# Kernel tuning notes

Measured on AMD Instinct MI355X. Metric: run time of the kernel, lower is better.

Reference implementation:

```python
import jax, jax.numpy as jnp
import numpy as np

E = 256      # embed_dim
H = 4        # num_heads
EXP = 4      # expansion_factor
B, C, R = 8, 32, 255  # batch, max_cols, rows (seq = R+1 with CLS)
LN_EPS = 1e-5


def setup_inputs() -> dict:
    key = jax.random.key(0)
    ks = jax.random.split(key, 16)
    s = 0.02
    return {
        "x": jax.random.normal(ks[0], (B, C, R, E), jnp.float32),
        "real_cols": jax.random.randint(ks[1], (B,), 0, C + 1),
        "real_rows": jax.random.randint(ks[2], (B,), 0, R + 1),
        "cls_token": jax.random.normal(ks[3], (E,), jnp.float32) * s,
        # MHA in_proj (torch packs q,k,v as (3E, E)) and out_proj
        "w_qkv": jax.random.normal(ks[4], (3 * E, E), jnp.float32) * s,
        "b_qkv": jnp.zeros((3 * E,), jnp.float32),
        "w_out": jax.random.normal(ks[5], (E, E), jnp.float32) * s,
        "b_out": jnp.zeros((E,), jnp.float32),
        # LayerNorm
        "ln_g": jnp.ones((E,), jnp.float32),
        "ln_b": jnp.zeros((E,), jnp.float32),
        # FFN: Linear(E, 4E) -> ReLU -> Linear(4E, E)
        "w1": jax.random.normal(ks[6], (EXP * E, E), jnp.float32) * s,
        "b1": jnp.zeros((EXP * E,), jnp.float32),
        "w2": jax.random.normal(ks[7], (E, EXP * E), jnp.float32) * s,
        "b2": jnp.zeros((E,), jnp.float32),
    }


def reference(x, real_cols, real_rows, cls_token, w_qkv, b_qkv, w_out, b_out,
              ln_g, ln_b, w1, b1, w2, b2):
    Bn, Cn, Rn, En = x.shape
    S = Rn + 1
    Dh = En // H
    dt = x.dtype

    # prepend CLS token to every column's row sequence -> (B, C, S, E)
    cls = jnp.broadcast_to(cls_token.astype(dt), (Bn, Cn, 1, En))
    xc = jnp.concatenate([cls, x], axis=2)

    # fused qkv projection
    qkv = jnp.einsum('bcse,fe->bcsf', xc, w_qkv.astype(dt)) + b_qkv.astype(dt)
    q, k, v = jnp.split(qkv, 3, axis=-1)
    q = q.reshape(Bn, Cn, S, H, Dh)
    k = k.reshape(Bn, Cn, S, H, Dh)
    v = v.reshape(Bn, Cn, S, H, Dh)

    scale = 1.0 / np.sqrt(Dh).astype(np.float32)
    scores = jnp.einsum('bcqhd,bckhd->bchqk', q, k) * scale  # (B,C,H,S,S)

    # key_padding_mask: position 0 (CLS) always valid; row p (1..R) valid iff p <= nrow
    pos = jnp.arange(S)
    valid = (pos[None, :] == 0) | (pos[None, :] <= real_rows[:, None])  # (B, S)
    neg = jnp.asarray(-1e9, scores.dtype)
    scores = jnp.where(valid[:, None, None, None, :], scores, neg)

    attn = jax.nn.softmax(scores, axis=-1)
    ctx = jnp.einsum('bchqk,bckhd->bcqhd', attn, v).reshape(Bn, Cn, S, En)
    mha = jnp.einsum('bcse,fe->bcsf', ctx, w_out.astype(dt)) + b_out.astype(dt)

    # LayerNorm over E
    mu = mha.mean(axis=-1, keepdims=True)
    var = ((mha - mu) ** 2).mean(axis=-1, keepdims=True)
    ln = (mha - mu) * jax.lax.rsqrt(var + LN_EPS) * ln_g.astype(dt) + ln_b.astype(dt)

    # FFN with residual from ln (out = ln + ffn(ln))
    h = jax.nn.relu(jnp.einsum('bcse,fe->bcsf', ln, w1.astype(dt)) + b1.astype(dt))
    ffn = jnp.einsum('bcsf,ef->bcse', h, w2.astype(dt)) + b2.astype(dt)
    out = ln + ffn

    # rep_mode == 'cls': take CLS position; zero out padded columns
    rep = out[:, :, 0, :]  # (B, C, E)
    col_valid = (jnp.arange(Cn)[None, :] < real_cols[:, None]).astype(dt)
    return rep * col_valid[..., None]
```

## Files before the change

### kernel.cpp

```cpp
#include <hip/hip_runtime.h>
#include <hip/hip_bf16.h>
#include <math.h>

static constexpr int kC = 32, kR = 255, kE = 256;

__device__ float g_vc[256];
__device__ float g_qw[4 * 256];
__device__ float g_s0[4];
__device__ float g_qb[4];
__device__ float g_m[256 * 4 * 4];
__device__ float g_l[256 * 4 * 4];
__device__ float g_part[256 * 4 * 4 * 256];
__device__ float g_ln[256 * 256];
__device__ float g_hact[256 * 1024];
__device__ unsigned short g_wv_bf[256 * 256];
__device__ unsigned short g_wout_bf[256 * 256];
__device__ unsigned short g_w1_bf[1024 * 256];
__device__ unsigned short g_w2_bf[256 * 1024];

__device__ inline unsigned short f2bf(float f) {
  __hip_bfloat16 h = __float2bfloat16(f);
  return __builtin_bit_cast(unsigned short, h);
}
__device__ inline float bflo(unsigned int u) { return __uint_as_float(u << 16); }
__device__ inline float bfhi(unsigned int u) { return __uint_as_float(u & 0xffff0000u); }

__global__ __launch_bounds__(256) void k_setup(const float* __restrict__ cls,
                                               const float* __restrict__ w_qkv,
                                               const float* __restrict__ b_qkv,
                                               const float* __restrict__ w_out,
                                               const float* __restrict__ w1,
                                               const float* __restrict__ w2) {
  const int t = threadIdx.x;
  if (blockIdx.x >= 4) {
    const int u = blockIdx.x - 4;
    const float* src;
    unsigned short* dst;
    size_t base;
    if (u < 64) { src = w_qkv + 512 * 256; dst = g_wv_bf; base = (size_t)u * 1024; }
    else if (u < 128) { src = w_out; dst = g_wout_bf; base = (size_t)(u - 64) * 1024; }
    else if (u < 384) { src = w1; dst = g_w1_bf; base = (size_t)(u - 128) * 1024; }
    else { src = w2; dst = g_w2_bf; base = (size_t)(u - 384) * 1024; }
    const size_t idx = base + (size_t)t * 4;
    float4 v = *(const float4*)(src + idx);
    ushort4 o;
    o.x = f2bf(v.x); o.y = f2bf(v.y); o.z = f2bf(v.z); o.w = f2bf(v.w);
    *(ushort4*)(dst + idx) = o;
    return;
  }

  const int h = blockIdx.x;
  __shared__ float clss[256], q0s[256];
  clss[t] = cls[t];
  __syncthreads();
  {
    float acc = b_qkv[t];
    const float4* wr = (const float4*)(w_qkv + (size_t)t * 256);
    const float4* c4 = (const float4*)clss;
#pragma unroll 8
    for (int e4 = 0; e4 < 64; ++e4) {
      float4 w4 = wr[e4], v4 = c4[e4];
      acc += w4.x * v4.x + w4.y * v4.y + w4.z * v4.z + w4.w * v4.w;
    }
    q0s[t] = acc;
  }
  __syncthreads();
  {
    float acc = 0.f;
#pragma unroll 8
    for (int j = 0; j < 64; ++j)
      acc += q0s[h * 64 + j] * w_qkv[(size_t)(256 + h * 64 + j) * 256 + t];
    g_qw[h * 256 + t] = acc * 0.125f;
  }
  if (t < 64) {
    const int row = 256 + h * 64 + t;
    float kc = b_qkv[row];
    const float4* wr = (const float4*)(w_qkv + (size_t)row * 256);
    const float4* c4 = (const float4*)clss;
#pragma unroll 8
    for (int e4 = 0; e4 < 64; ++e4) {
      float4 w4 = wr[e4], v4 = c4[e4];
      kc += w4.x * v4.x + w4.y * v4.y + w4.z * v4.z + w4.w * v4.w;
    }
    const float q = q0s[h * 64 + t];
    float pk = q * kc, pb = q * b_qkv[row];
#pragma unroll
    for (int m = 1; m < 64; m <<= 1) {
      pk += __shfl_xor(pk, m);
      pb += __shfl_xor(pb, m);
    }
    if (t == 0) {
      g_s0[h] = pk * 0.125f;
      g_qb[h] = pb * 0.125f;
    }
  } else if (t < 128) {
    const int f = h * 64 + (t - 64);
    const int row = 512 + f;
    float acc = b_qkv[row];
    const float4* wr = (const float4*)(w_qkv + (size_t)row * 256);
    const float4* c4 = (const float4*)clss;
#pragma unroll 8
    for (int e4 = 0; e4 < 64; ++e4) {
      float4 w4 = wr[e4], v4 = c4[e4];
      acc += w4.x * v4.x + w4.y * v4.y + w4.z * v4.z + w4.w * v4.w;
    }
    g_vc[f] = acc;
  }
}

__global__ __launch_bounds__(256) void k_attn(const float* __restrict__ x,
                                              const int* __restrict__ real_cols,
                                              const int* __restrict__ real_rows) {
  const int bc = blockIdx.x, chunk = blockIdx.y;
  const int b = bc >> 5, c = bc & 31;
  if (c >= real_cols[b]) return;
  const int rr = real_rows[b];
  const int r0 = chunk * 64;
  const int nr = min(64, rr - r0);
  if (nr <= 0) return;

  __shared__ float xs[64][260];
  __shared__ float qws[4][256];
  __shared__ float ps[4][64];
  const int t = threadIdx.x, wv = t >> 6, l = t & 63;

#pragma unroll
  for (int i = 0; i < 4; ++i) qws[i][t] = g_qw[i * 256 + t];

  const float* xb = x + ((size_t)bc * kR + r0) * kE;
  for (int r = wv; r < nr; r += 4)
    *(float4*)&xs[r][4 * l] = *(const float4*)(xb + (size_t)r * kE + 4 * l);
  __syncthreads();

  const int h = wv, row = l;
  float acc = 0.f;
  const float4* qrow = (const float4*)&qws[h][0];
  const float4* xrow = (const float4*)&xs[row][0];
#pragma unroll 8
  for (int e4 = 0; e4 < 64; ++e4) {
    float4 q4 = qrow[e4];
    float4 x4 = xrow[e4];
    acc += q4.x * x4.x + q4.y * x4.y + q4.z * x4.z + q4.w * x4.w;
  }
  float s = (row < nr) ? acc + g_qb[h] : -1e30f;
  float mx = s;
#pragma unroll
  for (int m = 1; m < 64; m <<= 1) mx = fmaxf(mx, __shfl_xor(mx, m));
  float p = (row < nr) ? __expf(s - mx) : 0.f;
  float lsum = p;
#pragma unroll
  for (int m = 1; m < 64; m <<= 1) lsum += __shfl_xor(lsum, m);
  ps[h][row] = p;
  if (l == 0) {
    g_m[(bc * 4 + chunk) * 4 + h] = mx;
    g_l[(bc * 4 + chunk) * 4 + h] = lsum;
  }
  __syncthreads();

  float a0 = 0.f, a1 = 0.f, a2 = 0.f, a3 = 0.f;
  for (int r2 = 0; r2 < nr; ++r2) {
    float xv = xs[r2][t];
    a0 += ps[0][r2] * xv;
    a1 += ps[1][r2] * xv;
    a2 += ps[2][r2] * xv;
    a3 += ps[3][r2] * xv;
  }
  float* pp = g_part + (size_t)(bc * 4 + chunk) * 4 * 256;
  pp[0 * 256 + t] = a0;
  pp[1 * 256 + t] = a1;
  pp[2 * 256 + t] = a2;
  pp[3 * 256 + t] = a3;
}

__global__ __launch_bounds__(256) void k_tail(const int* __restrict__ real_cols,
                                              const int* __restrict__ real_rows,
                                              const float* __restrict__ b_qkv,
                                              const float* __restrict__ b_out,
                                              const float* __restrict__ ln_g,
                                              const float* __restrict__ ln_b) {
  const int bc = blockIdx.x, b = bc >> 5, c = bc & 31;
  if (c >= real_cols[b]) return;
  const int rr = real_rows[b];
  const int nch = (rr + 63) >> 6;
  const int t = threadIdx.x, wv = t >> 6, l = t & 63;

  __shared__ float xb[4][256];
  __shared__ float ctxs[256];
  __shared__ float al[4][4];
  __shared__ float p0s[4];
  __shared__ float rb[2][4];

  if (t < 4) {
    const int h = t;
    const float s0 = g_s0[h];
    float M = s0;
    for (int ch = 0; ch < nch; ++ch) M = fmaxf(M, g_m[(bc * 4 + ch) * 4 + h]);
    float lt = __expf(s0 - M);
    const float w0 = lt;
    float av[4] = {0.f, 0.f, 0.f, 0.f};
    for (int ch = 0; ch < nch; ++ch) {
      float e = __expf(g_m[(bc * 4 + ch) * 4 + h] - M);
      av[ch] = e;
      lt += g_l[(bc * 4 + ch) * 4 + h] * e;
    }
    const float inv = 1.f / lt;
#pragma unroll
    for (int ch = 0; ch < 4; ++ch) al[h][ch] = av[ch] * inv;
    p0s[h] = w0 * inv;
  }
  __syncthreads();

#pragma unroll
  for (int h = 0; h < 4; ++h) {
    float a = 0.f;
    for (int ch = 0; ch < nch; ++ch)
      a += al[h][ch] * g_part[(size_t)(bc * 4 + ch) * 4 * 256 + h * 256 + t];
    xb[h][t] = a;
  }
  __syncthreads();

  {
    const int h = wv;
    const float p0 = p0s[h];
    float acc = p0 * g_vc[t] + (1.f - p0) * b_qkv[512 + t];
    const uint4* wr = (const uint4*)(g_wv_bf + (size_t)t * 256);
    const float4* v4p = (const float4*)&xb[h][0];
#pragma unroll 4
    for (int e8 = 0; e8 < 32; ++e8) {
      uint4 w = wr[e8];
      float4 a = v4p[2 * e8], bb = v4p[2 * e8 + 1];
      acc += bflo(w.x) * a.x + bfhi(w.x) * a.y + bflo(w.y) * a.z + bfhi(w.y) * a.w +
             bflo(w.z) * bb.x + bfhi(w.z) * bb.y + bflo(w.w) * bb.z + bfhi(w.w) * bb.w;
    }
    ctxs[t] = acc;
  }
  __syncthreads();

  float mh;
  {
    float acc = b_out[t];
    const uint4* wr = (const uint4*)(g_wout_bf + (size_t)t * 256);
    const float4* c4 = (const float4*)&ctxs[0];
#pragma unroll 4
    for (int e8 = 0; e8 < 32; ++e8) {
      uint4 w = wr[e8];
      float4 a = c4[2 * e8], bb = c4[2 * e8 + 1];
      acc += bflo(w.x) * a.x + bfhi(w.x) * a.y + bflo(w.y) * a.z + bfhi(w.y) * a.w +
             bflo(w.z) * bb.x + bfhi(w.z) * bb.y + bflo(w.w) * bb.z + bfhi(w.w) * bb.w;
    }
    mh = acc;
  }

  float s1 = mh, s2 = mh * mh;
#pragma unroll
  for (int m = 1; m < 64; m <<= 1) {
    s1 += __shfl_xor(s1, m);
    s2 += __shfl_xor(s2, m);
  }
  if (l == 0) {
    rb[0][wv] = s1;
    rb[1][wv] = s2;
  }
  __syncthreads();
  const float mu = (rb[0][0] + rb[0][1] + rb[0][2] + rb[0][3]) * (1.f / 256.f);
  const float msq = (rb[1][0] + rb[1][1] + rb[1][2] + rb[1][3]) * (1.f / 256.f);
  const float var = msq - mu * mu;
  g_ln[(size_t)bc * 256 + t] =
      (mh - mu) * rsqrtf(var + 1e-5f) * ln_g[t] + ln_b[t];
}

__global__ __launch_bounds__(256) void k_ffn1(const float* __restrict__ b1,
                                              const int* __restrict__ real_cols) {
  const int tok0 = blockIdx.x * 8;
  const int b = tok0 >> 5, c0 = tok0 & 31;
  if (c0 >= real_cols[b]) return;
  __shared__ float lns[8][256];
  const int t = threadIdx.x;
  const int f0 = blockIdx.y * 128;
#pragma unroll
  for (int i = 0; i < 8; ++i) lns[i][t] = g_ln[(size_t)(tok0 + i) * 256 + t];
  __syncthreads();
  const int f = f0 + (t & 127), half = t >> 7;
  const uint4* wr = (const uint4*)(g_w1_bf + (size_t)f * 256);
  const float bb = b1[f];
  float acc[4] = {bb, bb, bb, bb};
  for (int e8 = 0; e8 < 32; ++e8) {
    uint4 w = wr[e8];
    const float wv0 = bflo(w.x), wv1 = bfhi(w.x), wv2 = bflo(w.y), wv3 = bfhi(w.y);
    const float wv4 = bflo(w.z), wv5 = bfhi(w.z), wv6 = bflo(w.w), wv7 = bfhi(w.w);
#pragma unroll
    for (int k = 0; k < 4; ++k) {
      const int i = half * 4 + k;
      const float4 a = *(const float4*)&lns[i][8 * e8];
      const float4 bbv = *(const float4*)&lns[i][8 * e8 + 4];
      acc[k] += wv0 * a.x + wv1 * a.y + wv2 * a.z + wv3 * a.w +
                wv4 * bbv.x + wv5 * bbv.y + wv6 * bbv.z + wv7 * bbv.w;
    }
  }
#pragma unroll
  for (int k = 0; k < 4; ++k)
    g_hact[(size_t)(tok0 + half * 4 + k) * 1024 + f] = fmaxf(acc[k], 0.f);
}

__global__ __launch_bounds__(256) void k_ffn2(const float* __restrict__ b2,
                                              const int* __restrict__ real_cols,
                                              float* __restrict__ out) {
  const int t = threadIdx.x;
  const int tok0 = blockIdx.x * 8, e0 = blockIdx.y * 32;
  const int b = tok0 >> 5, c0 = tok0 & 31;
  const int ncols = real_cols[b];
  if (c0 >= ncols) {
    out[(size_t)(tok0 + (t >> 5)) * 256 + e0 + (t & 31)] = 0.f;
    return;
  }
  __shared__ float hs[8][1024];
#pragma unroll
  for (int i = 0; i < 8; ++i) {
#pragma unroll
    for (int j = 0; j < 4; ++j)
      hs[i][j * 256 + t] = g_hact[(size_t)(tok0 + i) * 1024 + j * 256 + t];
  }
  __syncthreads();
  const int e = e0 + (t & 31), i = t >> 5;
  const int tok = tok0 + i, c = tok & 31;
  const uint4* wr = (const uint4*)(g_w2_bf + (size_t)e * 1024);
  const float4* h4 = (const float4*)&hs[i][0];
  float acc = b2[e];
  for (int f8 = 0; f8 < 128; ++f8) {
    uint4 w = wr[f8];
    float4 a = h4[2 * f8], bb = h4[2 * f8 + 1];
    acc += bflo(w.x) * a.x + bfhi(w.x) * a.y + bflo(w.y) * a.z + bfhi(w.y) * a.w +
           bflo(w.z) * bb.x + bfhi(w.z) * bb.y + bflo(w.w) * bb.z + bfhi(w.w) * bb.w;
  }
  const float lnv = g_ln[(size_t)tok * 256 + e];
  out[(size_t)tok * 256 + e] = (c < ncols) ? (lnv + acc) : 0.f;
}

extern "C" void kernel_launch(void* const* d_in, const int* in_sizes, int n_in,
                              void* d_out, int out_size, void* d_ws, size_t ws_size,
                              hipStream_t stream) {
  const float* x = (const float*)d_in[0];
  const int* real_cols = (const int*)d_in[1];
  const int* real_rows = (const int*)d_in[2];
  const float* cls = (const float*)d_in[3];
  const float* w_qkv = (const float*)d_in[4];
  const float* b_qkv = (const float*)d_in[5];
  const float* w_out = (const float*)d_in[6];
  const float* b_out = (const float*)d_in[7];
  const float* ln_g = (const float*)d_in[8];
  const float* ln_b = (const float*)d_in[9];
  const float* w1 = (const float*)d_in[10];
  const float* b1 = (const float*)d_in[11];
  const float* w2 = (const float*)d_in[12];
  const float* b2 = (const float*)d_in[13];
  float* out = (float*)d_out;
  (void)in_sizes; (void)n_in; (void)out_size; (void)d_ws; (void)ws_size;

  k_setup<<<644, 256, 0, stream>>>(cls, w_qkv, b_qkv, w_out, w1, w2);
  k_attn<<<dim3(256, 4), 256, 0, stream>>>(x, real_cols, real_rows);
  k_tail<<<256, 256, 0, stream>>>(real_cols, real_rows, b_qkv, b_out, ln_g, ln_b);
  k_ffn1<<<dim3(32, 8), 256, 0, stream>>>(b1, real_cols);
  k_ffn2<<<dim3(32, 8), 256, 0, stream>>>(b2, real_cols, out);
}
```

Measured before the change: 185.3 us.

## Fuse setup/attn/tail into persistent ticket kernel and merge FFN stages with flags

Merges the setup, attention and tail kernels into one 1024-block kernel. Blocks prefetch their x tile, then take setup work items from an atomic ticket counter, and spin-wait on completion counters before attention. A last-arriver counter per (b,c) runs the tail. The two FFN kernels become one launch in which the ffn2 blocks spin on per-group counters written by the ffn1 blocks. This removes launch gaps and overlaps the weight casting with the x loads. It relies on all blocks being co-resident, so the spin-waits risk deadlock or stalls.

```diff
diff --git a/kernel.cpp b/kernel.cpp
--- a/kernel.cpp
+++ b/kernel.cpp
@@ -3,6 +3,13 @@
 #include <math.h>
 
 static constexpr int kC = 32, kR = 255, kE = 256;
+#define AGENT __HIP_MEMORY_SCOPE_AGENT
+
+__device__ unsigned g_ticket = 0;
+__device__ unsigned g_done_heads = 0;
+__device__ unsigned g_done_all = 0;
+__device__ unsigned g_bcnt[256];
+__device__ unsigned g_gcnt[32];
 
 __device__ float g_vc[256];
 __device__ float g_qw[4 * 256];
@@ -24,172 +31,199 @@
 }
 __device__ inline float bflo(unsigned int u) { return __uint_as_float(u << 16); }
 __device__ inline float bfhi(unsigned int u) { return __uint_as_float(u & 0xffff0000u); }
-
-__global__ __launch_bounds__(256) void k_setup(const float* __restrict__ cls,
-                                               const float* __restrict__ w_qkv,
-                                               const float* __restrict__ b_qkv,
-                                               const float* __restrict__ w_out,
-                                               const float* __restrict__ w1,
-                                               const float* __restrict__ w2) {
-  const int t = threadIdx.x;
-  if (blockIdx.x >= 4) {
-    const int u = blockIdx.x - 4;
-    const float* src;
-    unsigned short* dst;
-    size_t base;
-    if (u < 64) { src = w_qkv + 512 * 256; dst = g_wv_bf; base = (size_t)u * 1024; }
-    else if (u < 128) { src = w_out; dst = g_wout_bf; base = (size_t)(u - 64) * 1024; }
-    else if (u < 384) { src = w1; dst = g_w1_bf; base = (size_t)(u - 128) * 1024; }
-    else { src = w2; dst = g_w2_bf; base = (size_t)(u - 384) * 1024; }
-    const size_t idx = base + (size_t)t * 4;
-    float4 v = *(const float4*)(src + idx);
-    ushort4 o;
-    o.x = f2bf(v.x); o.y = f2bf(v.y); o.z = f2bf(v.z); o.w = f2bf(v.w);
-    *(ushort4*)(dst + idx) = o;
-    return;
-  }
-
-  const int h = blockIdx.x;
-  __shared__ float clss[256], q0s[256];
+__device__ inline unsigned aload(unsigned* p) {
+  return __hip_atomic_load(p, __ATOMIC_ACQUIRE, AGENT);
+}
+
+__device__ void do_head_item(int h, int t, int wv, int l, float* clss, float* q0h,
+                             float* kcs, const float* __restrict__ cls,
+                             const float* __restrict__ w_qkv,
+                             const float* __restrict__ b_qkv) {
   clss[t] = cls[t];
   __syncthreads();
-  {
-    float acc = b_qkv[t];
-    const float4* wr = (const float4*)(w_qkv + (size_t)t * 256);
-    const float4* c4 = (const float4*)clss;
-#pragma unroll 8
-    for (int e4 = 0; e4 < 64; ++e4) {
-      float4 w4 = wr[e4], v4 = c4[e4];
-      acc += w4.x * v4.x + w4.y * v4.y + w4.z * v4.z + w4.w * v4.w;
-    }
-    q0s[t] = acc;
+  const float4* c4 = (const float4*)clss;
+  for (int j = wv; j < 64; j += 4) {
+    const float4* wr = (const float4*)(w_qkv + (size_t)(h * 64 + j) * 256);
+    float4 w4 = wr[l], v4 = c4[l];
+    float a = w4.x * v4.x + w4.y * v4.y + w4.z * v4.z + w4.w * v4.w;
+#pragma unroll
+    for (int m = 1; m < 64; m <<= 1) a += __shfl_xor(a, m);
+    if (l == 0) q0h[j] = a + b_qkv[h * 64 + j];
   }
   __syncthreads();
   {
     float acc = 0.f;
 #pragma unroll 8
     for (int j = 0; j < 64; ++j)
-      acc += q0s[h * 64 + j] * w_qkv[(size_t)(256 + h * 64 + j) * 256 + t];
+      acc += q0h[j] * w_qkv[(size_t)(256 + h * 64 + j) * 256 + t];
     g_qw[h * 256 + t] = acc * 0.125f;
   }
-  if (t < 64) {
-    const int row = 256 + h * 64 + t;
-    float kc = b_qkv[row];
-    const float4* wr = (const float4*)(w_qkv + (size_t)row * 256);
-    const float4* c4 = (const float4*)clss;
-#pragma unroll 8
-    for (int e4 = 0; e4 < 64; ++e4) {
-      float4 w4 = wr[e4], v4 = c4[e4];
-      kc += w4.x * v4.x + w4.y * v4.y + w4.z * v4.z + w4.w * v4.w;
-    }
-    const float q = q0s[h * 64 + t];
-    float pk = q * kc, pb = q * b_qkv[row];
+  for (int j = wv; j < 64; j += 4) {
+    const float4* wr = (const float4*)(w_qkv + (size_t)(256 + h * 64 + j) * 256);
+    float4 w4 = wr[l], v4 = c4[l];
+    float a = w4.x * v4.x + w4.y * v4.y + w4.z * v4.z + w4.w * v4.w;
+#pragma unroll
+    for (int m = 1; m < 64; m <<= 1) a += __shfl_xor(a, m);
+    if (l == 0) kcs[j] = a + b_qkv[256 + h * 64 + j];
+  }
+  __syncthreads();
+  if (wv == 0) {
+    float q = q0h[l];
+    float pk = q * kcs[l], pb = q * b_qkv[256 + h * 64 + l];
 #pragma unroll
     for (int m = 1; m < 64; m <<= 1) {
       pk += __shfl_xor(pk, m);
       pb += __shfl_xor(pb, m);
     }
-    if (t == 0) {
+    if (l == 0) {
       g_s0[h] = pk * 0.125f;
       g_qb[h] = pb * 0.125f;
     }
-  } else if (t < 128) {
-    const int f = h * 64 + (t - 64);
-    const int row = 512 + f;
-    float acc = b_qkv[row];
-    const float4* wr = (const float4*)(w_qkv + (size_t)row * 256);
-    const float4* c4 = (const float4*)clss;
-#pragma unroll 8
-    for (int e4 = 0; e4 < 64; ++e4) {
-      float4 w4 = wr[e4], v4 = c4[e4];
-      acc += w4.x * v4.x + w4.y * v4.y + w4.z * v4.z + w4.w * v4.w;
-    }
-    g_vc[f] = acc;
-  }
-}
-
-__global__ __launch_bounds__(256) void k_attn(const float* __restrict__ x,
-                                              const int* __restrict__ real_cols,
-                                              const int* __restrict__ real_rows) {
-  const int bc = blockIdx.x, chunk = blockIdx.y;
+  }
+  for (int j = wv; j < 64; j += 4) {
+    const float4* wr = (const float4*)(w_qkv + (size_t)(512 + h * 64 + j) * 256);
+    float4 w4 = wr[l], v4 = c4[l];
+    float a = w4.x * v4.x + w4.y * v4.y + w4.z * v4.z + w4.w * v4.w;
+#pragma unroll
+    for (int m = 1; m < 64; m <<= 1) a += __shfl_xor(a, m);
+    if (l == 0) g_vc[h * 64 + j] = a + b_qkv[512 + h * 64 + j];
+  }
+}
+
+__device__ void do_cast_item(int u, int t, const float* __restrict__ w_qkv,
+                             const float* __restrict__ w_out,
+                             const float* __restrict__ w1,
+                             const float* __restrict__ w2) {
+  const float* src;
+  unsigned short* dst;
+  size_t base;
+  if (u < 64) { src = w_qkv + 512 * 256; dst = g_wv_bf; base = (size_t)u * 1024; }
+  else if (u < 128) { src = w_out; dst = g_wout_bf; base = (size_t)(u - 64) * 1024; }
+  else if (u < 384) { src = w1; dst = g_w1_bf; base = (size_t)(u - 128) * 1024; }
+  else { src = w2; dst = g_w2_bf; base = (size_t)(u - 384) * 1024; }
+  const size_t idx = base + (size_t)t * 4;
+  float4 v = *(const float4*)(src + idx);
+  ushort4 o;
+  o.x = f2bf(v.x); o.y = f2bf(v.y); o.z = f2bf(v.z); o.w = f2bf(v.w);
+  *(ushort4*)(dst + idx) = o;
+}
+
+__global__ __launch_bounds__(256) void k_fused(
+    const float* __restrict__ x, const int* __restrict__ real_cols,
+    const int* __restrict__ real_rows, const float* __restrict__ cls,
+    const float* __restrict__ w_qkv, const float* __restrict__ b_qkv,
+    const float* __restrict__ b_out, const float* __restrict__ ln_g,
+    const float* __restrict__ ln_b, const float* __restrict__ w_out,
+    const float* __restrict__ w1, const float* __restrict__ w2) {
+  const int t = threadIdx.x, wv = t >> 6, l = t & 63;
+  const int bid = blockIdx.x;
+  if (bid < 32 && t == 0) g_gcnt[bid] = 0;
+  const int bc = bid >> 2, chunk = bid & 3;
   const int b = bc >> 5, c = bc & 31;
-  if (c >= real_cols[b]) return;
-  const int rr = real_rows[b];
+  const int ncols = real_cols[b], rr = real_rows[b];
+  const bool bcvalid = (c < ncols);
   const int r0 = chunk * 64;
   const int nr = min(64, rr - r0);
-  if (nr <= 0) return;
 
   __shared__ float xs[64][260];
   __shared__ float qws[4][256];
   __shared__ float ps[4][64];
-  const int t = threadIdx.x, wv = t >> 6, l = t & 63;
-
-#pragma unroll
-  for (int i = 0; i < 4; ++i) qws[i][t] = g_qw[i * 256 + t];
-
-  const float* xb = x + ((size_t)bc * kR + r0) * kE;
-  for (int r = wv; r < nr; r += 4)
-    *(float4*)&xs[r][4 * l] = *(const float4*)(xb + (size_t)r * kE + 4 * l);
-  __syncthreads();
-
-  const int h = wv, row = l;
-  float acc = 0.f;
-  const float4* qrow = (const float4*)&qws[h][0];
-  const float4* xrow = (const float4*)&xs[row][0];
-#pragma unroll 8
-  for (int e4 = 0; e4 < 64; ++e4) {
-    float4 q4 = qrow[e4];
-    float4 x4 = xrow[e4];
-    acc += q4.x * x4.x + q4.y * x4.y + q4.z * x4.z + q4.w * x4.w;
-  }
-  float s = (row < nr) ? acc + g_qb[h] : -1e30f;
-  float mx = s;
-#pragma unroll
-  for (int m = 1; m < 64; m <<= 1) mx = fmaxf(mx, __shfl_xor(mx, m));
-  float p = (row < nr) ? __expf(s - mx) : 0.f;
-  float lsum = p;
-#pragma unroll
-  for (int m = 1; m < 64; m <<= 1) lsum += __shfl_xor(lsum, m);
-  ps[h][row] = p;
-  if (l == 0) {
-    g_m[(bc * 4 + chunk) * 4 + h] = mx;
-    g_l[(bc * 4 + chunk) * 4 + h] = lsum;
-  }
-  __syncthreads();
-
-  float a0 = 0.f, a1 = 0.f, a2 = 0.f, a3 = 0.f;
-  for (int r2 = 0; r2 < nr; ++r2) {
-    float xv = xs[r2][t];
-    a0 += ps[0][r2] * xv;
-    a1 += ps[1][r2] * xv;
-    a2 += ps[2][r2] * xv;
-    a3 += ps[3][r2] * xv;
-  }
-  float* pp = g_part + (size_t)(bc * 4 + chunk) * 4 * 256;
-  pp[0 * 256 + t] = a0;
-  pp[1 * 256 + t] = a1;
-  pp[2 * 256 + t] = a2;
-  pp[3 * 256 + t] = a3;
-}
-
-__global__ __launch_bounds__(256) void k_tail(const int* __restrict__ real_cols,
-                                              const int* __restrict__ real_rows,
-                                              const float* __restrict__ b_qkv,
-                                              const float* __restrict__ b_out,
-                                              const float* __restrict__ ln_g,
-                                              const float* __restrict__ ln_b) {
-  const int bc = blockIdx.x, b = bc >> 5, c = bc & 31;
-  if (c >= real_cols[b]) return;
-  const int rr = real_rows[b];
-  const int nch = (rr + 63) >> 6;
-  const int t = threadIdx.x, wv = t >> 6, l = t & 63;
-
+  __shared__ float clss[256], q0h[64], kcs[64];
   __shared__ float xb[4][256];
   __shared__ float ctxs[256];
   __shared__ float al[4][4];
   __shared__ float p0s[4];
   __shared__ float rb[2][4];
-
+  __shared__ unsigned sh_item;
+  __shared__ int sh_last;
+
+  if (bcvalid && nr > 0) {
+    const float* xp = x + ((size_t)bc * kR + r0) * kE;
+    for (int r = wv; r < nr; r += 4)
+      *(float4*)&xs[r][4 * l] = *(const float4*)(xp + (size_t)r * kE + 4 * l);
+  }
+
+  for (;;) {
+    __syncthreads();
+    if (t == 0)
+      sh_item = __hip_atomic_fetch_add(&g_ticket, 1u, __ATOMIC_RELAXED, AGENT);
+    __syncthreads();
+    const unsigned it = sh_item;
+    if (it >= 644u) break;
+    if (it < 4u) do_head_item((int)it, t, wv, l, clss, q0h, kcs, cls, w_qkv, b_qkv);
+    else do_cast_item((int)it - 4, t, w_qkv, w_out, w1, w2);
+    __threadfence();
+    __syncthreads();
+    if (t == 0) {
+      __hip_atomic_fetch_add(&g_done_all, 1u, __ATOMIC_RELEASE, AGENT);
+      if (it < 4u)
+        __hip_atomic_fetch_add(&g_done_heads, 1u, __ATOMIC_RELEASE, AGENT);
+    }
+  }
+
+  if (bcvalid && nr > 0) {
+    if (t == 0)
+      while (aload(&g_done_heads) < 4u) __builtin_amdgcn_s_sleep(2);
+    __syncthreads();
+    __threadfence();
+#pragma unroll
+    for (int i = 0; i < 4; ++i) qws[i][t] = g_qw[i * 256 + t];
+    __syncthreads();
+
+    const int h = wv, row = l;
+    float acc = 0.f;
+    const float4* qrow = (const float4*)&qws[h][0];
+    const float4* xrow = (const float4*)&xs[row][0];
+#pragma unroll 8
+    for (int e4 = 0; e4 < 64; ++e4) {
+      float4 q4 = qrow[e4], x4 = xrow[e4];
+      acc += q4.x * x4.x + q4.y * x4.y + q4.z * x4.z + q4.w * x4.w;
+    }
+    float s = (row < nr) ? acc + g_qb[h] : -1e30f;
+    float mx = s;
+#pragma unroll
+    for (int m = 1; m < 64; m <<= 1) mx = fmaxf(mx, __shfl_xor(mx, m));
+    float p = (row < nr) ? __expf(s - mx) : 0.f;
+    float lsum = p;
+#pragma unroll
+    for (int m = 1; m < 64; m <<= 1) lsum += __shfl_xor(lsum, m);
+    ps[h][row] = p;
+    if (l == 0) {
+      g_m[(bc * 4 + chunk) * 4 + h] = mx;
+      g_l[(bc * 4 + chunk) * 4 + h] = lsum;
+    }
+    __syncthreads();
+
+    float a0 = 0.f, a1 = 0.f, a2 = 0.f, a3 = 0.f;
+    for (int r2 = 0; r2 < nr; ++r2) {
+      float xv = xs[r2][t];
+      a0 += ps[0][r2] * xv;
+      a1 += ps[1][r2] * xv;
+      a2 += ps[2][r2] * xv;
+      a3 += ps[3][r2] * xv;
+    }
+    float* pp = g_part + (size_t)(bc * 4 + chunk) * 4 * 256;
+    pp[0 * 256 + t] = a0;
+    pp[1 * 256 + t] = a1;
+    pp[2 * 256 + t] = a2;
+    pp[3 * 256 + t] = a3;
+  }
+
+  __threadfence();
+  __syncthreads();
+  if (t == 0)
+    sh_last = (__hip_atomic_fetch_add(&g_bcnt[bc], 1u, __ATOMIC_ACQ_REL, AGENT) == 3u);
+  __syncthreads();
+  if (!sh_last) return;
+  if (t == 0) __hip_atomic_store(&g_bcnt[bc], 0u, __ATOMIC_RELAXED, AGENT);
+  if (!bcvalid) return;
+
+  if (t == 0)
+    while (aload(&g_done_all) < 644u) __builtin_amdgcn_s_sleep(2);
+  __syncthreads();
+  __threadfence();
+
+  const int nch = (rr + 63) >> 6;
   if (t < 4) {
     const int h = t;
     const float s0 = g_s0[h];
@@ -269,50 +303,67 @@
       (mh - mu) * rsqrtf(var + 1e-5f) * ln_g[t] + ln_b[t];
 }
 
-__global__ __launch_bounds__(256) void k_ffn1(const float* __restrict__ b1,
-                                              const int* __restrict__ real_cols) {
-  const int tok0 = blockIdx.x * 8;
-  const int b = tok0 >> 5, c0 = tok0 & 31;
-  if (c0 >= real_cols[b]) return;
-  __shared__ float lns[8][256];
+__global__ __launch_bounds__(256) void k_ffn(const float* __restrict__ b1,
+                                             const float* __restrict__ b2,
+                                             const int* __restrict__ real_cols,
+                                             float* __restrict__ out) {
   const int t = threadIdx.x;
-  const int f0 = blockIdx.y * 128;
-#pragma unroll
-  for (int i = 0; i < 8; ++i) lns[i][t] = g_ln[(size_t)(tok0 + i) * 256 + t];
-  __syncthreads();
-  const int f = f0 + (t & 127), half = t >> 7;
-  const uint4* wr = (const uint4*)(g_w1_bf + (size_t)f * 256);
-  const float bb = b1[f];
-  float acc[4] = {bb, bb, bb, bb};
-  for (int e8 = 0; e8 < 32; ++e8) {
-    uint4 w = wr[e8];
-    const float wv0 = bflo(w.x), wv1 = bfhi(w.x), wv2 = bflo(w.y), wv3 = bfhi(w.y);
-    const float wv4 = bflo(w.z), wv5 = bfhi(w.z), wv6 = bflo(w.w), wv7 = bfhi(w.w);
-#pragma unroll
-    for (int k = 0; k < 4; ++k) {
-      const int i = half * 4 + k;
-      const float4 a = *(const float4*)&lns[i][8 * e8];
-      const float4 bbv = *(const float4*)&lns[i][8 * e8 + 4];
-      acc[k] += wv0 * a.x + wv1 * a.y + wv2 * a.z + wv3 * a.w +
-                wv4 * bbv.x + wv5 * bbv.y + wv6 * bbv.z + wv7 * bbv.w;
-    }
-  }
-#pragma unroll
-  for (int k = 0; k < 4; ++k)
-    g_hact[(size_t)(tok0 + half * 4 + k) * 1024 + f] = fmaxf(acc[k], 0.f);
-}
-
-__global__ __launch_bounds__(256) void k_ffn2(const float* __restrict__ b2,
-                                              const int* __restrict__ real_cols,
-                                              float* __restrict__ out) {
-  const int t = threadIdx.x;
-  const int tok0 = blockIdx.x * 8, e0 = blockIdx.y * 32;
+  if (blockIdx.x == 0 && t == 0) {
+    g_ticket = 0;
+    g_done_heads = 0;
+    g_done_all = 0;
+  }
+
+  if (blockIdx.x < 256) {
+    const int g = blockIdx.x >> 3, f0 = (blockIdx.x & 7) * 128;
+    const int tok0 = g * 8;
+    const int b = tok0 >> 5, c0 = tok0 & 31;
+    if (c0 < real_cols[b]) {
+      __shared__ float lns[8][256];
+#pragma unroll
+      for (int i = 0; i < 8; ++i) lns[i][t] = g_ln[(size_t)(tok0 + i) * 256 + t];
+      __syncthreads();
+      const int f = f0 + (t & 127), half = t >> 7;
+      const uint4* wr = (const uint4*)(g_w1_bf + (size_t)f * 256);
+      const float bb = b1[f];
+      float acc[4] = {bb, bb, bb, bb};
+      for (int e8 = 0; e8 < 32; ++e8) {
+        uint4 w = wr[e8];
+        const float w0 = bflo(w.x), w1v = bfhi(w.x), w2v = bflo(w.y), w3 = bfhi(w.y);
+        const float w4v = bflo(w.z), w5 = bfhi(w.z), w6 = bflo(w.w), w7 = bfhi(w.w);
+#pragma unroll
+        for (int k = 0; k < 4; ++k) {
+          const int i = half * 4 + k;
+          const float4 a = *(const float4*)&lns[i][8 * e8];
+          const float4 bbv = *(const float4*)&lns[i][8 * e8 + 4];
+          acc[k] += w0 * a.x + w1v * a.y + w2v * a.z + w3 * a.w +
+                    w4v * bbv.x + w5 * bbv.y + w6 * bbv.z + w7 * bbv.w;
+        }
+      }
+#pragma unroll
+      for (int k = 0; k < 4; ++k)
+        g_hact[(size_t)(tok0 + half * 4 + k) * 1024 + f] = fmaxf(acc[k], 0.f);
+    }
+    __threadfence();
+    __syncthreads();
+    if (t == 0) __hip_atomic_fetch_add(&g_gcnt[g], 1u, __ATOMIC_RELEASE, AGENT);
+    return;
+  }
+
+  const int jj = blockIdx.x - 256;
+  const int g = jj >> 3, e0 = (jj & 7) * 32;
+  const int tok0 = g * 8;
   const int b = tok0 >> 5, c0 = tok0 & 31;
   const int ncols = real_cols[b];
   if (c0 >= ncols) {
     out[(size_t)(tok0 + (t >> 5)) * 256 + e0 + (t & 31)] = 0.f;
     return;
   }
+  if (t == 0)
+    while (aload(&g_gcnt[g]) < 8u) __builtin_amdgcn_s_sleep(2);
+  __syncthreads();
+  __threadfence();
+
   __shared__ float hs[8][1024];
 #pragma unroll
   for (int i = 0; i < 8; ++i) {
@@ -356,9 +407,7 @@
   float* out = (float*)d_out;
   (void)in_sizes; (void)n_in; (void)out_size; (void)d_ws; (void)ws_size;
 
-  k_setup<<<644, 256, 0, stream>>>(cls, w_qkv, b_qkv, w_out, w1, w2);
-  k_attn<<<dim3(256, 4), 256, 0, stream>>>(x, real_cols, real_rows);
-  k_tail<<<256, 256, 0, stream>>>(real_cols, real_rows, b_qkv, b_out, ln_g, ln_b);
-  k_ffn1<<<dim3(32, 8), 256, 0, stream>>>(b1, real_cols);
-  k_ffn2<<<dim3(32, 8), 256, 0, stream>>>(b2, real_cols, out);
-}
+  k_fused<<<1024, 256, 0, stream>>>(x, real_cols, real_rows, cls, w_qkv, b_qkv,
+                                    b_out, ln_g, ln_b, w_out, w1, w2);
+  k_ffn<<<512, 256, 0, stream>>>(b1, b2, real_cols, out);
+}
```

Result: slower. 734.6 us (+296.5%).

## Fuse tail, FFN1 and FFN2 into one per-token kernel

Applied to the files above, without the earlier changes.

Merges the LayerNorm tail and both FFN matmuls into a single kernel with one block per (batch, column) token. The LN output and hidden activation stay in shared memory, which removes two kernel launches and the global round-trips through g_ln and g_hact. In exchange, each block now streams the full bf16 W1 and W2 (about 1 MB) by itself. The earlier kernels shared each weight load across 8 tokens, so weight traffic per token rises, relying on L2 to absorb the reuse.

```diff
diff --git a/kernel.cpp b/kernel.cpp
--- a/kernel.cpp
+++ b/kernel.cpp
@@ -11,8 +11,6 @@
 __device__ float g_m[256 * 4 * 4];
 __device__ float g_l[256 * 4 * 4];
 __device__ float g_part[256 * 4 * 4 * 256];
-__device__ float g_ln[256 * 256];
-__device__ float g_hact[256 * 1024];
 __device__ unsigned short g_wv_bf[256 * 256];
 __device__ unsigned short g_wout_bf[256 * 256];
 __device__ unsigned short g_w1_bf[1024 * 256];
@@ -172,20 +170,26 @@
   pp[3 * 256 + t] = a3;
 }
 
-__global__ __launch_bounds__(256) void k_tail(const int* __restrict__ real_cols,
-                                              const int* __restrict__ real_rows,
-                                              const float* __restrict__ b_qkv,
-                                              const float* __restrict__ b_out,
-                                              const float* __restrict__ ln_g,
-                                              const float* __restrict__ ln_b) {
+__global__ __launch_bounds__(256) void k_tail_ffn(
+    const int* __restrict__ real_cols, const int* __restrict__ real_rows,
+    const float* __restrict__ b_qkv, const float* __restrict__ b_out,
+    const float* __restrict__ ln_g, const float* __restrict__ ln_b,
+    const float* __restrict__ b1, const float* __restrict__ b2,
+    float* __restrict__ out) {
   const int bc = blockIdx.x, b = bc >> 5, c = bc & 31;
-  if (c >= real_cols[b]) return;
+  const int t = threadIdx.x, wv = t >> 6, l = t & 63;
+  float* orow = out + (size_t)bc * kE;
+  if (c >= real_cols[b]) {
+    orow[t] = 0.f;
+    return;
+  }
   const int rr = real_rows[b];
   const int nch = (rr + 63) >> 6;
-  const int t = threadIdx.x, wv = t >> 6, l = t & 63;
 
   __shared__ float xb[4][256];
   __shared__ float ctxs[256];
+  __shared__ float lns[256];
+  __shared__ float hs[1024];
   __shared__ float al[4][4];
   __shared__ float p0s[4];
   __shared__ float rb[2][4];
@@ -265,75 +269,54 @@
   const float mu = (rb[0][0] + rb[0][1] + rb[0][2] + rb[0][3]) * (1.f / 256.f);
   const float msq = (rb[1][0] + rb[1][1] + rb[1][2] + rb[1][3]) * (1.f / 256.f);
   const float var = msq - mu * mu;
-  g_ln[(size_t)bc * 256 + t] =
-      (mh - mu) * rsqrtf(var + 1e-5f) * ln_g[t] + ln_b[t];
-}
-
-__global__ __launch_bounds__(256) void k_ffn1(const float* __restrict__ b1,
-                                              const int* __restrict__ real_cols) {
-  const int tok0 = blockIdx.x * 8;
-  const int b = tok0 >> 5, c0 = tok0 & 31;
-  if (c0 >= real_cols[b]) return;
-  __shared__ float lns[8][256];
-  const int t = threadIdx.x;
-  const int f0 = blockIdx.y * 128;
-#pragma unroll
-  for (int i = 0; i < 8; ++i) lns[i][t] = g_ln[(size_t)(tok0 + i) * 256 + t];
-  __syncthreads();
-  const int f = f0 + (t & 127), half = t >> 7;
-  const uint4* wr = (const uint4*)(g_w1_bf + (size_t)f * 256);
-  const float bb = b1[f];
-  float acc[4] = {bb, bb, bb, bb};
-  for (int e8 = 0; e8 < 32; ++e8) {
-    uint4 w = wr[e8];
-    const float wv0 = bflo(w.x), wv1 = bfhi(w.x), wv2 = bflo(w.y), wv3 = bfhi(w.y);
-    const float wv4 = bflo(w.z), wv5 = bfhi(w.z), wv6 = bflo(w.w), wv7 = bfhi(w.w);
-#pragma unroll
-    for (int k = 0; k < 4; ++k) {
-      const int i = half * 4 + k;
-      const float4 a = *(const float4*)&lns[i][8 * e8];
-      const float4 bbv = *(const float4*)&lns[i][8 * e8 + 4];
-      acc[k] += wv0 * a.x + wv1 * a.y + wv2 * a.z + wv3 * a.w +
-                wv4 * bbv.x + wv5 * bbv.y + wv6 * bbv.z + wv7 * bbv.w;
-    }
-  }
-#pragma unroll
-  for (int k = 0; k < 4; ++k)
-    g_hact[(size_t)(tok0 + half * 4 + k) * 1024 + f] = fmaxf(acc[k], 0.f);
-}
-
-__global__ __launch_bounds__(256) void k_ffn2(const float* __restrict__ b2,
-                                              const int* __restrict__ real_cols,
-                                              float* __restrict__ out) {
-  const int t = threadIdx.x;
-  const int tok0 = blockIdx.x * 8, e0 = blockIdx.y * 32;
-  const int b = tok0 >> 5, c0 = tok0 & 31;
-  const int ncols = real_cols[b];
-  if (c0 >= ncols) {
-    out[(size_t)(tok0 + (t >> 5)) * 256 + e0 + (t & 31)] = 0.f;
-    return;
-  }
-  __shared__ float hs[8][1024];
-#pragma unroll
-  for (int i = 0; i < 8; ++i) {
-#pragma unroll
-    for (int j = 0; j < 4; ++j)
-      hs[i][j * 256 + t] = g_hact[(size_t)(tok0 + i) * 1024 + j * 256 + t];
-  }
-  __syncthreads();
-  const int e = e0 + (t & 31), i = t >> 5;
-  const int tok = tok0 + i, c = tok & 31;
-  const uint4* wr = (const uint4*)(g_w2_bf + (size_t)e * 1024);
-  const float4* h4 = (const float4*)&hs[i][0];
-  float acc = b2[e];
-  for (int f8 = 0; f8 < 128; ++f8) {
-    uint4 w = wr[f8];
-    float4 a = h4[2 * f8], bb = h4[2 * f8 + 1];
-    acc += bflo(w.x) * a.x + bfhi(w.x) * a.y + bflo(w.y) * a.z + bfhi(w.y) * a.w +
-           bflo(w.z) * bb.x + bfhi(w.z) * bb.y + bflo(w.w) * bb.z + bfhi(w.w) * bb.w;
-  }
-  const float lnv = g_ln[(size_t)tok * 256 + e];
-  out[(size_t)tok * 256 + e] = (c < ncols) ? (lnv + acc) : 0.f;
+  const float lnv = (mh - mu) * rsqrtf(var + 1e-5f) * ln_g[t] + ln_b[t];
+  lns[t] = lnv;
+  __syncthreads();
+
+  {
+    float acc0 = b1[t], acc1 = b1[t + 256], acc2 = b1[t + 512], acc3 = b1[t + 768];
+    const uint4* w0r = (const uint4*)(g_w1_bf + (size_t)t * 256);
+    const uint4* w1r = (const uint4*)(g_w1_bf + (size_t)(t + 256) * 256);
+    const uint4* w2r = (const uint4*)(g_w1_bf + (size_t)(t + 512) * 256);
+    const uint4* w3r = (const uint4*)(g_w1_bf + (size_t)(t + 768) * 256);
+    const float4* l4 = (const float4*)&lns[0];
+#pragma unroll 2
+    for (int e8 = 0; e8 < 32; ++e8) {
+      const float4 a = l4[2 * e8], bb = l4[2 * e8 + 1];
+      uint4 w;
+      w = w0r[e8];
+      acc0 += bflo(w.x) * a.x + bfhi(w.x) * a.y + bflo(w.y) * a.z + bfhi(w.y) * a.w +
+              bflo(w.z) * bb.x + bfhi(w.z) * bb.y + bflo(w.w) * bb.z + bfhi(w.w) * bb.w;
+      w = w1r[e8];
+      acc1 += bflo(w.x) * a.x + bfhi(w.x) * a.y + bflo(w.y) * a.z + bfhi(w.y) * a.w +
+              bflo(w.z) * bb.x + bfhi(w.z) * bb.y + bflo(w.w) * bb.z + bfhi(w.w) * bb.w;
+      w = w2r[e8];
+      acc2 += bflo(w.x) * a.x + bfhi(w.x) * a.y + bflo(w.y) * a.z + bfhi(w.y) * a.w +
+              bflo(w.z) * bb.x + bfhi(w.z) * bb.y + bflo(w.w) * bb.z + bfhi(w.w) * bb.w;
+      w = w3r[e8];
+      acc3 += bflo(w.x) * a.x + bfhi(w.x) * a.y + bflo(w.y) * a.z + bfhi(w.y) * a.w +
+              bflo(w.z) * bb.x + bfhi(w.z) * bb.y + bflo(w.w) * bb.z + bfhi(w.w) * bb.w;
+    }
+    hs[t] = fmaxf(acc0, 0.f);
+    hs[t + 256] = fmaxf(acc1, 0.f);
+    hs[t + 512] = fmaxf(acc2, 0.f);
+    hs[t + 768] = fmaxf(acc3, 0.f);
+  }
+  __syncthreads();
+
+  {
+    float acc = b2[t];
+    const uint4* wr = (const uint4*)(g_w2_bf + (size_t)t * 1024);
+    const float4* h4 = (const float4*)&hs[0];
+#pragma unroll 4
+    for (int f8 = 0; f8 < 128; ++f8) {
+      uint4 w = wr[f8];
+      float4 a = h4[2 * f8], bb = h4[2 * f8 + 1];
+      acc += bflo(w.x) * a.x + bfhi(w.x) * a.y + bflo(w.y) * a.z + bfhi(w.y) * a.w +
+             bflo(w.z) * bb.x + bfhi(w.z) * bb.y + bflo(w.w) * bb.z + bfhi(w.w) * bb.w;
+    }
+    orow[t] = lnv + acc;
+  }
 }
 
 extern "C" void kernel_launch(void* const* d_in, const int* in_sizes, int n_in,
@@ -358,7 +341,6 @@
 
   k_setup<<<644, 256, 0, stream>>>(cls, w_qkv, b_qkv, w_out, w1, w2);
   k_attn<<<dim3(256, 4), 256, 0, stream>>>(x, real_cols, real_rows);
-  k_tail<<<256, 256, 0, stream>>>(real_cols, real_rows, b_qkv, b_out, ln_g, ln_b);
-  k_ffn1<<<dim3(32, 8), 256, 0, stream>>>(b1, real_cols);
-  k_ffn2<<<dim3(32, 8), 256, 0, stream>>>(b2, real_cols, out);
-}
+  k_tail_ffn<<<256, 256, 0, stream>>>(real_cols, real_rows, b_qkv, b_out,
+                                      ln_g, ln_b, b1, b2, out);
+}
```

New measurement: 189.6 us. 1.02x slower.

## Store bf16 weights in k-chunk-major layout for coalesced GEMV loads; parallelize setup dots

Applied to the files above, without the earlier changes.

The setup kernel now writes the bf16 copies of the V, out-proj, W1 and W2 weights in a chunked layout where each 8-element k-chunk is contiguous across output rows. Consecutive threads therefore read adjacent 16-byte words instead of strided row starts. The consuming GEMV loops in the attention, ffn1 and ffn2 kernels index the new layout. The CLS q/k/v projections in setup now use one wavefront per row with shuffle reductions, replacing one thread per row with long serial loops. This changes the layout contract between kernels, so every consumer must agree with it.

```diff
diff --git a/kernel.cpp b/kernel.cpp
--- a/kernel.cpp
+++ b/kernel.cpp
@@ -31,80 +31,65 @@
                                                const float* __restrict__ w_out,
                                                const float* __restrict__ w1,
                                                const float* __restrict__ w2) {
-  const int t = threadIdx.x;
+  const int t = threadIdx.x, wvi = t >> 6, l = t & 63;
   if (blockIdx.x >= 4) {
     const int u = blockIdx.x - 4;
     const float* src;
     unsigned short* dst;
-    size_t base;
-    if (u < 64) { src = w_qkv + 512 * 256; dst = g_wv_bf; base = (size_t)u * 1024; }
-    else if (u < 128) { src = w_out; dst = g_wout_bf; base = (size_t)(u - 64) * 1024; }
-    else if (u < 384) { src = w1; dst = g_w1_bf; base = (size_t)(u - 128) * 1024; }
-    else { src = w2; dst = g_w2_bf; base = (size_t)(u - 384) * 1024; }
-    const size_t idx = base + (size_t)t * 4;
+    int OUT, insh;
+    size_t idx0;
+    if (u < 64) { src = w_qkv + 512 * 256; dst = g_wv_bf; OUT = 256; insh = 8; idx0 = (size_t)u * 1024; }
+    else if (u < 128) { src = w_out; dst = g_wout_bf; OUT = 256; insh = 8; idx0 = (size_t)(u - 64) * 1024; }
+    else if (u < 384) { src = w1; dst = g_w1_bf; OUT = 1024; insh = 8; idx0 = (size_t)(u - 128) * 1024; }
+    else { src = w2; dst = g_w2_bf; OUT = 256; insh = 10; idx0 = (size_t)(u - 384) * 1024; }
+    const size_t idx = idx0 + (size_t)t * 4;
+    const int o = (int)(idx >> insh), e = (int)(idx & ((1 << insh) - 1));
     float4 v = *(const float4*)(src + idx);
-    ushort4 o;
-    o.x = f2bf(v.x); o.y = f2bf(v.y); o.z = f2bf(v.z); o.w = f2bf(v.w);
-    *(ushort4*)(dst + idx) = o;
+    ushort4 ov;
+    ov.x = f2bf(v.x); ov.y = f2bf(v.y); ov.z = f2bf(v.z); ov.w = f2bf(v.w);
+    *(ushort4*)(dst + ((size_t)(e >> 3) * OUT + o) * 8 + (e & 7)) = ov;
     return;
   }
 
   const int h = blockIdx.x;
-  __shared__ float clss[256], q0s[256];
+  __shared__ float clss[256], q0h[64], kch[64];
   clss[t] = cls[t];
   __syncthreads();
-  {
-    float acc = b_qkv[t];
-    const float4* wr = (const float4*)(w_qkv + (size_t)t * 256);
-    const float4* c4 = (const float4*)clss;
-#pragma unroll 8
-    for (int e4 = 0; e4 < 64; ++e4) {
-      float4 w4 = wr[e4], v4 = c4[e4];
-      acc += w4.x * v4.x + w4.y * v4.y + w4.z * v4.z + w4.w * v4.w;
-    }
-    q0s[t] = acc;
+  const float4 c4v = *((const float4*)clss + l);
+  for (int r = wvi; r < 192; r += 4) {
+    const int kind = r >> 6, j = r & 63;
+    const int row = kind * 256 + h * 64 + j;
+    const float4 w4 = *((const float4*)(w_qkv + (size_t)row * 256) + l);
+    float a = w4.x * c4v.x + w4.y * c4v.y + w4.z * c4v.z + w4.w * c4v.w;
+#pragma unroll
+    for (int m = 1; m < 64; m <<= 1) a += __shfl_xor(a, m);
+    if (l == 0) {
+      const float val = a + b_qkv[row];
+      if (kind == 0) q0h[j] = val;
+      else if (kind == 1) kch[j] = val;
+      else g_vc[h * 64 + j] = val;
+    }
   }
   __syncthreads();
   {
     float acc = 0.f;
 #pragma unroll 8
     for (int j = 0; j < 64; ++j)
-      acc += q0s[h * 64 + j] * w_qkv[(size_t)(256 + h * 64 + j) * 256 + t];
+      acc += q0h[j] * w_qkv[(size_t)(256 + h * 64 + j) * 256 + t];
     g_qw[h * 256 + t] = acc * 0.125f;
   }
-  if (t < 64) {
-    const int row = 256 + h * 64 + t;
-    float kc = b_qkv[row];
-    const float4* wr = (const float4*)(w_qkv + (size_t)row * 256);
-    const float4* c4 = (const float4*)clss;
-#pragma unroll 8
-    for (int e4 = 0; e4 < 64; ++e4) {
-      float4 w4 = wr[e4], v4 = c4[e4];
-      kc += w4.x * v4.x + w4.y * v4.y + w4.z * v4.z + w4.w * v4.w;
-    }
-    const float q = q0s[h * 64 + t];
-    float pk = q * kc, pb = q * b_qkv[row];
+  if (wvi == 0) {
+    const float q = q0h[l];
+    float pk = q * kch[l], pb = q * b_qkv[256 + h * 64 + l];
 #pragma unroll
     for (int m = 1; m < 64; m <<= 1) {
       pk += __shfl_xor(pk, m);
       pb += __shfl_xor(pb, m);
     }
-    if (t == 0) {
+    if (l == 0) {
       g_s0[h] = pk * 0.125f;
       g_qb[h] = pb * 0.125f;
     }
-  } else if (t < 128) {
-    const int f = h * 64 + (t - 64);
-    const int row = 512 + f;
-    float acc = b_qkv[row];
-    const float4* wr = (const float4*)(w_qkv + (size_t)row * 256);
-    const float4* c4 = (const float4*)clss;
-#pragma unroll 8
-    for (int e4 = 0; e4 < 64; ++e4) {
-      float4 w4 = wr[e4], v4 = c4[e4];
-      acc += w4.x * v4.x + w4.y * v4.y + w4.z * v4.z + w4.w * v4.w;
-    }
-    g_vc[f] = acc;
   }
 }
 
@@ -223,11 +208,11 @@
     const int h = wv;
     const float p0 = p0s[h];
     float acc = p0 * g_vc[t] + (1.f - p0) * b_qkv[512 + t];
-    const uint4* wr = (const uint4*)(g_wv_bf + (size_t)t * 256);
+    const uint4* wr = (const uint4*)g_wv_bf;
     const float4* v4p = (const float4*)&xb[h][0];
 #pragma unroll 4
     for (int e8 = 0; e8 < 32; ++e8) {
-      uint4 w = wr[e8];
+      uint4 w = wr[e8 * 256 + t];
       float4 a = v4p[2 * e8], bb = v4p[2 * e8 + 1];
       acc += bflo(w.x) * a.x + bfhi(w.x) * a.y + bflo(w.y) * a.z + bfhi(w.y) * a.w +
              bflo(w.z) * bb.x + bfhi(w.z) * bb.y + bflo(w.w) * bb.z + bfhi(w.w) * bb.w;
@@ -239,11 +224,11 @@
   float mh;
   {
     float acc = b_out[t];
-    const uint4* wr = (const uint4*)(g_wout_bf + (size_t)t * 256);
+    const uint4* wr = (const uint4*)g_wout_bf;
     const float4* c4 = (const float4*)&ctxs[0];
 #pragma unroll 4
     for (int e8 = 0; e8 < 32; ++e8) {
-      uint4 w = wr[e8];
+      uint4 w = wr[e8 * 256 + t];
       float4 a = c4[2 * e8], bb = c4[2 * e8 + 1];
       acc += bflo(w.x) * a.x + bfhi(w.x) * a.y + bflo(w.y) * a.z + bfhi(w.y) * a.w +
              bflo(w.z) * bb.x + bfhi(w.z) * bb.y + bflo(w.w) * bb.z + bfhi(w.w) * bb.w;
@@ -281,20 +266,20 @@
   for (int i = 0; i < 8; ++i) lns[i][t] = g_ln[(size_t)(tok0 + i) * 256 + t];
   __syncthreads();
   const int f = f0 + (t & 127), half = t >> 7;
-  const uint4* wr = (const uint4*)(g_w1_bf + (size_t)f * 256);
+  const uint4* wr = (const uint4*)g_w1_bf;
   const float bb = b1[f];
   float acc[4] = {bb, bb, bb, bb};
   for (int e8 = 0; e8 < 32; ++e8) {
-    uint4 w = wr[e8];
-    const float wv0 = bflo(w.x), wv1 = bfhi(w.x), wv2 = bflo(w.y), wv3 = bfhi(w.y);
-    const float wv4 = bflo(w.z), wv5 = bfhi(w.z), wv6 = bflo(w.w), wv7 = bfhi(w.w);
+    uint4 w = wr[e8 * 1024 + f];
+    const float w0 = bflo(w.x), w1v = bfhi(w.x), w2v = bflo(w.y), w3 = bfhi(w.y);
+    const float w4v = bflo(w.z), w5 = bfhi(w.z), w6 = bflo(w.w), w7 = bfhi(w.w);
 #pragma unroll
     for (int k = 0; k < 4; ++k) {
       const int i = half * 4 + k;
       const float4 a = *(const float4*)&lns[i][8 * e8];
       const float4 bbv = *(const float4*)&lns[i][8 * e8 + 4];
-      acc[k] += wv0 * a.x + wv1 * a.y + wv2 * a.z + wv3 * a.w +
-                wv4 * bbv.x + wv5 * bbv.y + wv6 * bbv.z + wv7 * bbv.w;
+      acc[k] += w0 * a.x + w1v * a.y + w2v * a.z + w3 * a.w +
+                w4v * bbv.x + w5 * bbv.y + w6 * bbv.z + w7 * bbv.w;
     }
   }
 #pragma unroll
@@ -323,11 +308,11 @@
   __syncthreads();
   const int e = e0 + (t & 31), i = t >> 5;
   const int tok = tok0 + i, c = tok & 31;
-  const uint4* wr = (const uint4*)(g_w2_bf + (size_t)e * 1024);
+  const uint4* wr = (const uint4*)g_w2_bf;
   const float4* h4 = (const float4*)&hs[i][0];
   float acc = b2[e];
   for (int f8 = 0; f8 < 128; ++f8) {
-    uint4 w = wr[f8];
+    uint4 w = wr[f8 * 256 + e];
     float4 a = h4[2 * f8], bb = h4[2 * f8 + 1];
     acc += bflo(w.x) * a.x + bfhi(w.x) * a.y + bflo(w.y) * a.z + bfhi(w.y) * a.w +
            bflo(w.z) * bb.x + bfhi(w.z) * bb.y + bflo(w.w) * bb.z + bfhi(w.w) * bb.w;
```

After: 203.5 us. 9.9% more time.
